# Optimization experiments

Hardware: AMD Instinct MI355X
Metric: run time of the kernel (lower is better)

## Reference

```python
import jax, jax.numpy as jnp
import numpy as np

B, CIN, COUT, K, STRIDE, PAD = 32, 64, 128, 3, 1, 1
IN_H, IN_W = 112, 112


def setup_inputs() -> dict:
    key = jax.random.key(0)
    k1, k2 = jax.random.split(key)
    # x_padded already has `PAD` rows/cols of zeros on each side, as in the torch module
    x = jax.random.normal(k1, (B, CIN, IN_H, IN_W), dtype=jnp.float32)
    x_padded = jnp.pad(x, ((0, 0), (0, 0), (PAD, PAD), (PAD, PAD)))
    weight = jax.random.normal(k2, (COUT, CIN, K, K), dtype=jnp.float32) * 0.1
    bias = jnp.zeros((COUT,), dtype=jnp.float32)
    return {
        "x_padded": x_padded,
        "in_height": IN_H,
        "in_width": IN_W,
        "weight": weight,
        "bias": bias,
    }


def reference(x_padded, in_height, in_width, weight, bias):
    # CustomConv2D.custom_conv2d: direct conv over the pre-padded input.
    # out[b,o,h,w] = sum_{i,kh,kw} x_padded[b,i,h*s+kh,w*s+kw] * weight[o,i,kh,kw] + bias[o]
    out = jax.lax.conv_general_dilated(
        x_padded, weight,
        window_strides=(STRIDE, STRIDE),
        padding="VALID",  # padding already applied to x_padded
        dimension_numbers=("NCHW", "OIHW", "NCHW"),
    )
    return out + bias[None, :, None, None]
```

## Files before the change

kernel.cpp:

```cpp
#include <hip/hip_runtime.h>

typedef __attribute__((ext_vector_type(8))) short short8;
typedef __attribute__((ext_vector_type(4))) float f32x4;
typedef __attribute__((ext_vector_type(4))) unsigned int u32x4;
typedef unsigned short u16;
typedef unsigned int u32;
typedef unsigned long long u64;

#define XH 114
#define XW 114
#define CINC 64
#define COUT 128
#define OH 112
#define OW 112
#define NB 32
#define KTOT 576
#define TILEB 58368

static __device__ __forceinline__ u16 f2bf(float f) {
    u32 x = __float_as_uint(f);
    u32 r = (x + 0x7fffu + ((x >> 16) & 1u)) >> 16;
    return (u16)r;
}

#define MFMA16(a, b, c) __builtin_amdgcn_mfma_f32_16x16x32_bf16((a), (b), (c), 0, 0, 0)

static __device__ __forceinline__ void gload16(const void* g, void* l) {
    __builtin_amdgcn_global_load_lds(
        (const __attribute__((address_space(1))) unsigned int*)g,
        (__attribute__((address_space(3))) unsigned int*)l, 16, 0, 0);
}


__global__ __launch_bounds__(256) void wcvt_reord(const float* __restrict__ w,
                                                  u16* __restrict__ wbf) {
    int i = blockIdx.x * 256 + threadIdx.x;
    int o = i / KTOT;
    int rem = i - o * KTOT;
    int khkw = rem >> 6;
    int ci = rem & 63;
    wbf[i] = f2bf(w[(o * CINC + ci) * 9 + khkw]);
}

__global__ __launch_bounds__(256) void xcvt(const float* __restrict__ x,
                                            u16* __restrict__ xb) {
    __shared__ u16 tile[XW * 70];
    const int blk = blockIdx.x;
    const int b = blk / XH;
    const int h = blk - b * XH;
    const int tid = threadIdx.x;

    #pragma unroll
    for (int it = 0; it < 15; ++it) {
        int idx = it * 256 + tid;
        if (idx < 32 * XW) {
            int cp = idx / XW;
            int w_ = idx - cp * XW;
            const float* s0 = x + ((size_t)(b * CINC + 2 * cp) * XH + h) * XW + w_;
            float a = s0[0];
            float c = s0[XH * XW];
            u32 pk = (u32)f2bf(a) | ((u32)f2bf(c) << 16);
            *(u32*)&tile[w_ * 70 + 2 * cp] = pk;
        }
    }
    __syncthreads();

    u16* dstrow = xb + (size_t)(b * XH + h) * (XW * CINC);
    #pragma unroll
    for (int p2 = 0; p2 < 4; ++p2) {
        int task = p2 * 256 + tid;
        if (task < XW * 8) {
            int w_ = task >> 3;
            int c8 = task & 7;
            const u32* s = (const u32*)&tile[w_ * 70 + c8 * 8];
            u32x4 v = {s[0], s[1], s[2], s[3]};
            int slot = c8 ^ ((2 * h + w_) & 7);
            *(u32x4*)(dstrow + w_ * CINC + slot * 8) = v;
        }
    }
}

__global__ __launch_bounds__(512, 2) void conv_pers(const u16* __restrict__ xb,
                                                    const u16* __restrict__ wbf,
                                                    const float* __restrict__ bias,
                                                    float* __restrict__ out) {
    __shared__ u16 lds[2 * 4 * XW * CINC];
    char* ldsc = (char*)lds;

    const int tid  = threadIdx.x;
    const int lane = tid & 63;
    const int wv   = tid >> 6;
    const int l16  = lane & 15;
    const int lhi  = lane >> 4;
    const int wm   = wv & 3;
    const int wn   = wv >> 2;

    const int t0g = blockIdx.x * 7;

    const u16* wrow0 = wbf + (wm * 32 + l16) * KTOT + lhi * 8;
    const u16* wrow1 = wrow0 + 16 * KTOT;
    short8 areg[18][2];
    #pragma unroll
    for (int t = 0; t < 18; ++t) {
        areg[t][0] = *(const short8*)(wrow0 + t * 32);
        areg[t][1] = *(const short8*)(wrow1 + t * 32);
    }

    {
        const char* src = (const char*)(xb + (size_t)((t0g / 56) * XH + (t0g % 56) * 2) * (XW * CINC));
        #pragma unroll
        for (int it = 0; it < 8; ++it) {
            int off = it * 8192 + wv * 1024;
            if (off < TILEB) gload16(src + off + lane * 16, ldsc + off);
        }
    }

    const f32x4 zero = {0.f, 0.f, 0.f, 0.f};

    #pragma unroll 1
    for (int i = 0; i < 7; ++i) {
        __syncthreads();

        if (i < 6) {
            const int tg = t0g + i + 1;
            const char* src = (const char*)(xb + (size_t)((tg / 56) * XH + (tg % 56) * 2) * (XW * CINC));
            char* dstb = ldsc + ((i + 1) & 1) * TILEB;
            #pragma unroll
            for (int it = 0; it < 8; ++it) {
                int off = it * 8192 + wv * 1024;
                if (off < TILEB) gload16(src + off + lane * 16, dstb + off);
            }
        }

        const int tg = t0g + i;
        const int b  = tg / 56;
        const int h0 = (tg - b * 56) * 2;
        char* buf = ldsc + (i & 1) * TILEB;

        f32x4 acc[2][7];
        #pragma unroll
        for (int mf = 0; mf < 2; ++mf)
            #pragma unroll
            for (int nf = 0; nf < 7; ++nf) acc[mf][nf] = zero;

        #pragma unroll
        for (int tt = 0; tt < 9; ++tt) {
            const int kh = tt / 3;
            const int kw = tt - kh * 3;
            const int r  = wn + kh;
            const int pix0 = r * XW + kw + l16;
            const int hash = (2 * (h0 + r) + kw + l16) & 7;
            const int ba0 = (pix0 << 7) + ((lhi ^ hash) << 4);

            __builtin_amdgcn_s_setprio(1);
            #pragma unroll
            for (int nf = 0; nf < 7; ++nf) {
                short8 bf = *(const short8*)(buf + ba0 + nf * 2048);
                acc[0][nf] = MFMA16(areg[2 * tt][0], bf, acc[0][nf]);
                acc[1][nf] = MFMA16(areg[2 * tt][1], bf, acc[1][nf]);
            }
            __builtin_amdgcn_s_setprio(0);

            __builtin_amdgcn_s_setprio(1);
            #pragma unroll
            for (int nf = 0; nf < 7; ++nf) {
                short8 bf = *(const short8*)(buf + (ba0 ^ 0x40) + nf * 2048);
                acc[0][nf] = MFMA16(areg[2 * tt + 1][0], bf, acc[0][nf]);
                acc[1][nf] = MFMA16(areg[2 * tt + 1][1], bf, acc[1][nf]);
            }
            __builtin_amdgcn_s_setprio(0);
        }

        float* outb = out + (size_t)b * COUT * (OH * OW) + (h0 + wn) * OW;
        #pragma unroll
        for (int mf = 0; mf < 2; ++mf) {
            #pragma unroll
            for (int j = 0; j < 4; ++j) {
                const int o = wm * 32 + mf * 16 + lhi * 4 + j;
                const float bv = bias[o];
                #pragma unroll
                for (int nf = 0; nf < 7; ++nf) {
                    outb[(size_t)o * (OH * OW) + nf * 16 + l16] = acc[mf][nf][j] + bv;
                }
            }
        }
    }
}


#define BK 32
#define NSTEP 18
#define LDB 40

__global__ __launch_bounds__(256) void wcvt_ident(const float* __restrict__ w,
                                                  u16* __restrict__ wbf) {
    int i = blockIdx.x * 256 + threadIdx.x;
    if (i < COUT * KTOT) wbf[i] = f2bf(w[i]);
}

__global__ __launch_bounds__(256) void conv_fb(const float* __restrict__ x,
                                               const u16* __restrict__ wbf,
                                               const float* __restrict__ bias,
                                               float* __restrict__ out) {
    __shared__ u16 ldsB[OW * LDB];
    const int tid = threadIdx.x;
    int bid = blockIdx.x;
    { int xcd = bid & 7; bid = xcd * 448 + (bid >> 3); }
    const int b = bid / OH;
    const int h = bid - b * OH;
    const float* xbp = x + (size_t)b * (CINC * XH * XW);
    float* outb = out + (size_t)b * (COUT * OH * OW) + h * OW;
    const int lane = tid & 63, wv = tid >> 6, l16 = lane & 15, lhi = lane >> 4;
    const int m0 = wv * 32;
    const int sk = tid >> 3, sn0 = (tid & 7) * 14;
    f32x4 acc[2][7];
    const f32x4 zero = {0.f, 0.f, 0.f, 0.f};
    #pragma unroll
    for (int i = 0; i < 2; ++i)
        #pragma unroll
        for (int j = 0; j < 7; ++j) acc[i][j] = zero;
    for (int t = 0; t < NSTEP; ++t) {
        const int kg = t * BK + sk;
        const int ci = kg / 9;
        const int r9 = kg - ci * 9;
        const int kh = r9 / 3, kw = r9 - (r9 / 3) * 3;
        const float* src = xbp + ((size_t)ci * XH + (h + kh)) * XW + kw + sn0;
        __syncthreads();
        #pragma unroll
        for (int i = 0; i < 14; ++i) ldsB[(sn0 + i) * LDB + sk] = f2bf(src[i]);
        __syncthreads();
        short8 afrag[2];
        #pragma unroll
        for (int mf = 0; mf < 2; ++mf)
            afrag[mf] = *(const short8*)(wbf + (m0 + mf * 16 + l16) * KTOT + t * BK + lhi * 8);
        #pragma unroll
        for (int nf = 0; nf < 7; ++nf) {
            short8 bfrag = *(const short8*)&ldsB[(nf * 16 + l16) * LDB + lhi * 8];
            acc[0][nf] = MFMA16(afrag[0], bfrag, acc[0][nf]);
            acc[1][nf] = MFMA16(afrag[1], bfrag, acc[1][nf]);
        }
    }
    #pragma unroll
    for (int mf = 0; mf < 2; ++mf)
        #pragma unroll
        for (int j = 0; j < 4; ++j) {
            const int o = m0 + mf * 16 + lhi * 4 + j;
            const float bv = bias[o];
            #pragma unroll
            for (int nf = 0; nf < 7; ++nf)
                outb[(size_t)o * (OH * OW) + nf * 16 + l16] = acc[mf][nf][j] + bv;
        }
}

extern "C" void kernel_launch(void* const* d_in, const int* in_sizes, int n_in,
                              void* d_out, int out_size, void* d_ws, size_t ws_size,
                              hipStream_t stream) {
    const float* x    = (const float*)d_in[0];
    const float* w    = (const float*)d_in[3];
    const float* bias = (const float*)d_in[4];
    float* out = (float*)d_out;

    const size_t WBYTES = (size_t)COUT * KTOT * 2;
    const size_t XBYTES = (size_t)NB * XH * XW * CINC * 2;
    if (ws_size >= WBYTES + XBYTES) {
        u16* wbf = (u16*)d_ws;
        u16* xb  = (u16*)((char*)d_ws + WBYTES);
        wcvt_reord<<<(COUT * KTOT) / 256, 256, 0, stream>>>(w, wbf);
        xcvt<<<NB * XH, 256, 0, stream>>>(x, xb);
        conv_pers<<<256, 512, 0, stream>>>(xb, wbf, bias, out);
    } else {
        u16* wbf = (u16*)d_ws;
        wcvt_ident<<<(COUT * KTOT + 255) / 256, 256, 0, stream>>>(w, wbf);
        conv_fb<<<NB * OH, 256, 0, stream>>>(x, wbf, bias, out);
    }
}
```

Measured before the change: 122.1 us.

## Fuse input bf16 conversion into persistent conv kernel staging

Removes the separate xcvt pass that wrote a bf16 NHWC copy of the input to workspace; the conv kernel now reads fp32 NCHW rows directly, converts them to bf16 and writes them swizzled into LDS. Staging is split so half the waves stage before compute and half after, to overlap the conversion with MFMA work. MFMA operands are swapped so each lane holds 4 contiguous output pixels, allowing vectorized float4 stores, and block indices are remapped across XCDs. This saves a full write and re-read of the converted input, but staging now uses synchronous VALU loads and LDS stores in place of async global-to-LDS copies, which can stall compute.

```diff
diff --git a/kernel.cpp b/kernel.cpp
--- a/kernel.cpp
+++ b/kernel.cpp
@@ -2,10 +2,8 @@
 
 typedef __attribute__((ext_vector_type(8))) short short8;
 typedef __attribute__((ext_vector_type(4))) float f32x4;
-typedef __attribute__((ext_vector_type(4))) unsigned int u32x4;
 typedef unsigned short u16;
 typedef unsigned int u32;
-typedef unsigned long long u64;
 
 #define XH 114
 #define XW 114
@@ -25,13 +23,6 @@
 
 #define MFMA16(a, b, c) __builtin_amdgcn_mfma_f32_16x16x32_bf16((a), (b), (c), 0, 0, 0)
 
-static __device__ __forceinline__ void gload16(const void* g, void* l) {
-    __builtin_amdgcn_global_load_lds(
-        (const __attribute__((address_space(1))) unsigned int*)g,
-        (__attribute__((address_space(3))) unsigned int*)l, 16, 0, 0);
-}
-
-
 __global__ __launch_bounds__(256) void wcvt_reord(const float* __restrict__ w,
                                                   u16* __restrict__ wbf) {
     int i = blockIdx.x * 256 + threadIdx.x;
@@ -42,48 +33,10 @@
     wbf[i] = f2bf(w[(o * CINC + ci) * 9 + khkw]);
 }
 
-__global__ __launch_bounds__(256) void xcvt(const float* __restrict__ x,
-                                            u16* __restrict__ xb) {
-    __shared__ u16 tile[XW * 70];
-    const int blk = blockIdx.x;
-    const int b = blk / XH;
-    const int h = blk - b * XH;
-    const int tid = threadIdx.x;
-
-    #pragma unroll
-    for (int it = 0; it < 15; ++it) {
-        int idx = it * 256 + tid;
-        if (idx < 32 * XW) {
-            int cp = idx / XW;
-            int w_ = idx - cp * XW;
-            const float* s0 = x + ((size_t)(b * CINC + 2 * cp) * XH + h) * XW + w_;
-            float a = s0[0];
-            float c = s0[XH * XW];
-            u32 pk = (u32)f2bf(a) | ((u32)f2bf(c) << 16);
-            *(u32*)&tile[w_ * 70 + 2 * cp] = pk;
-        }
-    }
-    __syncthreads();
-
-    u16* dstrow = xb + (size_t)(b * XH + h) * (XW * CINC);
-    #pragma unroll
-    for (int p2 = 0; p2 < 4; ++p2) {
-        int task = p2 * 256 + tid;
-        if (task < XW * 8) {
-            int w_ = task >> 3;
-            int c8 = task & 7;
-            const u32* s = (const u32*)&tile[w_ * 70 + c8 * 8];
-            u32x4 v = {s[0], s[1], s[2], s[3]};
-            int slot = c8 ^ ((2 * h + w_) & 7);
-            *(u32x4*)(dstrow + w_ * CINC + slot * 8) = v;
-        }
-    }
-}
-
-__global__ __launch_bounds__(512, 2) void conv_pers(const u16* __restrict__ xb,
-                                                    const u16* __restrict__ wbf,
-                                                    const float* __restrict__ bias,
-                                                    float* __restrict__ out) {
+__global__ __launch_bounds__(512, 2) void conv_direct(const float* __restrict__ x,
+                                                      const u16* __restrict__ wbf,
+                                                      const float* __restrict__ bias,
+                                                      float* __restrict__ out) {
     __shared__ u16 lds[2 * 4 * XW * CINC];
     char* ldsc = (char*)lds;
 
@@ -95,7 +48,9 @@
     const int wm   = wv & 3;
     const int wn   = wv >> 2;
 
-    const int t0g = blockIdx.x * 7;
+    int bidx = blockIdx.x;
+    { int xcd = bidx & 7; bidx = xcd * 32 + (bidx >> 3); }
+    const int t0g = bidx * 7;
 
     const u16* wrow0 = wbf + (wm * 32 + l16) * KTOT + lhi * 8;
     const u16* wrow1 = wrow0 + 16 * KTOT;
@@ -106,36 +61,42 @@
         areg[t][1] = *(const short8*)(wrow1 + t * 32);
     }
 
-    {
-        const char* src = (const char*)(xb + (size_t)((t0g / 56) * XH + (t0g % 56) * 2) * (XW * CINC));
-        #pragma unroll
-        for (int it = 0; it < 8; ++it) {
-            int off = it * 8192 + wv * 1024;
-            if (off < TILEB) gload16(src + off + lane * 16, ldsc + off);
-        }
-    }
+    auto STAGE = [&](int tg, int bufsel) {
+        const int bb  = tg / 56;
+        const int hh0 = (tg - bb * 56) * 2;
+        char* dst = ldsc + bufsel * TILEB;
+        const int r  = wv >> 1;
+        const int cp0 = (wv & 1) * 16;
+        const float* xrow = x + ((size_t)(bb * CINC) * XH + (hh0 + r)) * XW;
+        const int hb = 2 * (hh0 + r);
+        #pragma unroll
+        for (int k = 0; k < 16; ++k) {
+            const int cp = cp0 + k;
+            const float* r0 = xrow + (size_t)(2 * cp) * (XH * XW);
+            const float* r1 = r0 + XH * XW;
+            const int slotb = cp >> 2;
+            const int cilo  = ((2 * cp) & 7) << 1;
+            {
+                const int w = lane;
+                u32 pk = (u32)f2bf(r0[w]) | ((u32)f2bf(r1[w]) << 16);
+                const int swz = slotb ^ ((hb + w) & 7);
+                *(u32*)(dst + ((((r * XW + w) << 7) | (swz << 4) | cilo))) = pk;
+            }
+            if (lane < XW - 64) {
+                const int w = 64 + lane;
+                u32 pk = (u32)f2bf(r0[w]) | ((u32)f2bf(r1[w]) << 16);
+                const int swz = slotb ^ ((hb + w) & 7);
+                *(u32*)(dst + ((((r * XW + w) << 7) | (swz << 4) | cilo))) = pk;
+            }
+        }
+    };
 
     const f32x4 zero = {0.f, 0.f, 0.f, 0.f};
 
-    #pragma unroll 1
-    for (int i = 0; i < 7; ++i) {
-        __syncthreads();
-
-        if (i < 6) {
-            const int tg = t0g + i + 1;
-            const char* src = (const char*)(xb + (size_t)((tg / 56) * XH + (tg % 56) * 2) * (XW * CINC));
-            char* dstb = ldsc + ((i + 1) & 1) * TILEB;
-            #pragma unroll
-            for (int it = 0; it < 8; ++it) {
-                int off = it * 8192 + wv * 1024;
-                if (off < TILEB) gload16(src + off + lane * 16, dstb + off);
-            }
-        }
-
-        const int tg = t0g + i;
-        const int b  = tg / 56;
-        const int h0 = (tg - b * 56) * 2;
-        char* buf = ldsc + (i & 1) * TILEB;
+    auto COMPUTE = [&](int tg, int bufsel) {
+        const int bb  = tg / 56;
+        const int hh0 = (tg - bb * 56) * 2;
+        char* buf = ldsc + bufsel * TILEB;
 
         f32x4 acc[2][7];
         #pragma unroll
@@ -149,15 +110,15 @@
             const int kw = tt - kh * 3;
             const int r  = wn + kh;
             const int pix0 = r * XW + kw + l16;
-            const int hash = (2 * (h0 + r) + kw + l16) & 7;
+            const int hash = (2 * (hh0 + r) + kw + l16) & 7;
             const int ba0 = (pix0 << 7) + ((lhi ^ hash) << 4);
 
             __builtin_amdgcn_s_setprio(1);
             #pragma unroll
             for (int nf = 0; nf < 7; ++nf) {
                 short8 bf = *(const short8*)(buf + ba0 + nf * 2048);
-                acc[0][nf] = MFMA16(areg[2 * tt][0], bf, acc[0][nf]);
-                acc[1][nf] = MFMA16(areg[2 * tt][1], bf, acc[1][nf]);
+                acc[0][nf] = MFMA16(bf, areg[2 * tt][0], acc[0][nf]);
+                acc[1][nf] = MFMA16(bf, areg[2 * tt][1], acc[1][nf]);
             }
             __builtin_amdgcn_s_setprio(0);
 
@@ -165,25 +126,35 @@
             #pragma unroll
             for (int nf = 0; nf < 7; ++nf) {
                 short8 bf = *(const short8*)(buf + (ba0 ^ 0x40) + nf * 2048);
-                acc[0][nf] = MFMA16(areg[2 * tt + 1][0], bf, acc[0][nf]);
-                acc[1][nf] = MFMA16(areg[2 * tt + 1][1], bf, acc[1][nf]);
+                acc[0][nf] = MFMA16(bf, areg[2 * tt + 1][0], acc[0][nf]);
+                acc[1][nf] = MFMA16(bf, areg[2 * tt + 1][1], acc[1][nf]);
             }
             __builtin_amdgcn_s_setprio(0);
         }
 
-        float* outb = out + (size_t)b * COUT * (OH * OW) + (h0 + wn) * OW;
         #pragma unroll
         for (int mf = 0; mf < 2; ++mf) {
-            #pragma unroll
-            for (int j = 0; j < 4; ++j) {
-                const int o = wm * 32 + mf * 16 + lhi * 4 + j;
-                const float bv = bias[o];
-                #pragma unroll
-                for (int nf = 0; nf < 7; ++nf) {
-                    outb[(size_t)o * (OH * OW) + nf * 16 + l16] = acc[mf][nf][j] + bv;
-                }
-            }
-        }
+            const int o = wm * 32 + mf * 16 + l16;
+            const float bv = bias[o];
+            float* po = out + ((size_t)bb * COUT + o) * (OH * OW) + (hh0 + wn) * OW;
+            #pragma unroll
+            for (int nf = 0; nf < 7; ++nf) {
+                f32x4 v = acc[mf][nf];
+                v[0] += bv; v[1] += bv; v[2] += bv; v[3] += bv;
+                *(f32x4*)(po + nf * 16 + lhi * 4) = v;
+            }
+        }
+    };
+
+    STAGE(t0g, 0);
+
+    #pragma unroll 1
+    for (int i = 0; i < 7; ++i) {
+        __syncthreads();
+        const bool sfirst = (wv < 4);
+        if (i < 6 && sfirst) STAGE(t0g + i + 1, (i + 1) & 1);
+        COMPUTE(t0g + i, i & 1);
+        if (i < 6 && !sfirst) STAGE(t0g + i + 1, (i + 1) & 1);
     }
 }
 
@@ -261,13 +232,10 @@
     float* out = (float*)d_out;
 
     const size_t WBYTES = (size_t)COUT * KTOT * 2;
-    const size_t XBYTES = (size_t)NB * XH * XW * CINC * 2;
-    if (ws_size >= WBYTES + XBYTES) {
+    if (ws_size >= WBYTES) {
         u16* wbf = (u16*)d_ws;
-        u16* xb  = (u16*)((char*)d_ws + WBYTES);
         wcvt_reord<<<(COUT * KTOT) / 256, 256, 0, stream>>>(w, wbf);
-        xcvt<<<NB * XH, 256, 0, stream>>>(x, xb);
-        conv_pers<<<256, 512, 0, stream>>>(xb, wbf, bias, out);
+        conv_direct<<<256, 512, 0, stream>>>(x, wbf, bias, out);
     } else {
         u16* wbf = (u16*)d_ws;
         wcvt_ident<<<(COUT * KTOT + 255) / 256, 256, 0, stream>>>(w, wbf);
```

Result: slower. 191.0 us (+56.4%).
